# Kernel optimization log

Measured on AMD Instinct MI355X. Metric: run time of the kernel, lower is better.

## Reference

```python
import jax, jax.numpy as jnp
import numpy as np

N_HEADS = 16
D_QK = 64
D_MODEL = 1024
LN_EPS = 1e-6
B, QL, KVL = 2, 2048, 2048


def rms_norm(x, weight, eps=LN_EPS):
    var = jnp.mean(jnp.square(x.astype(jnp.float32)), axis=-1, keepdims=True)
    return (x * jax.lax.rsqrt(var + eps)).astype(x.dtype) * weight


def setup_inputs() -> dict:
    key = jax.random.key(0)
    ks = jax.random.split(key, 5)
    scale_h = 1.0 / np.sqrt(D_MODEL)
    return {
        "q_hidden_states": jax.random.normal(ks[0], (B, QL, D_MODEL), jnp.float32),
        "q_sequence_mask": jnp.ones((B, QL), dtype=bool),
        "kv_hidden_states": jax.random.normal(ks[1], (B, KVL, D_MODEL), jnp.float32),
        "kv_sequence_mask": jnp.ones((B, KVL), dtype=bool),
        "w_q": jax.random.normal(ks[2], (D_MODEL, N_HEADS * D_QK), jnp.float32) * scale_h,
        "w_kv": jax.random.normal(ks[3], (D_MODEL, 2 * N_HEADS * D_QK), jnp.float32) * scale_h,
        "w_o": jax.random.normal(ks[4], (N_HEADS * D_QK, D_MODEL), jnp.float32) * scale_h,
        "ln_weight": jnp.ones((D_MODEL,), jnp.float32),
    }


def reference(q_hidden_states, q_sequence_mask, kv_hidden_states, kv_sequence_mask,
              w_q, w_kv, w_o, ln_weight):
    b, ql, _ = q_hidden_states.shape
    kvl = kv_hidden_states.shape[1]

    normed = rms_norm(q_hidden_states, ln_weight)

    # q projection: [b, ql, H*D] -> [b, H, ql, D]
    q = (normed @ w_q).reshape(b, ql, N_HEADS, D_QK).transpose(0, 2, 1, 3)
    # kv projection: [b, kvl, 2*H*D] -> k, v each [b, H, kvl, D]
    kv = (kv_hidden_states @ w_kv).reshape(b, kvl, 2, N_HEADS, D_QK)
    k = kv[:, :, 0].transpose(0, 2, 1, 3)
    v = kv[:, :, 1].transpose(0, 2, 1, 3)

    # T5 attention: no 1/sqrt(d) scaling
    scores = jnp.einsum("bhqd,bhkd->bhqk", q, k)  # [b, H, ql, kvl]
    attn_mask = q_sequence_mask[:, None, :, None] & kv_sequence_mask[:, None, None, :]
    scores = jnp.where(attn_mask, scores, jnp.finfo(jnp.float32).min)
    attn = jax.nn.softmax(scores.astype(jnp.float32), axis=-1).astype(q.dtype)

    out = jnp.einsum("bhqk,bhkd->bhqd", attn, v)  # [b, H, ql, D]
    out = out.transpose(0, 2, 1, 3).reshape(b, ql, N_HEADS * D_QK)
    out = out @ w_o
    return q_hidden_states + out
```

## Files before the change

kernel.cpp:

```cpp
#include <hip/hip_runtime.h>
#include <stdint.h>

#define BSZ 2
#define QL 2048
#define KVL 2048
#define NH 16
#define DQK 64
#define DM 1024

typedef __bf16 bf16x8 __attribute__((ext_vector_type(8)));
typedef float f32x4 __attribute__((ext_vector_type(4)));

__device__ __forceinline__ ushort f2bf(float f) {
    union { float f; uint32_t u; } c; c.f = f;
    uint32_t u = c.u;
    return (ushort)((u + 0x7fffu + ((u >> 16) & 1u)) >> 16);
}

__device__ __forceinline__ uint32_t pack2bf(float lo, float hi) {
    union { float f; uint32_t u; } a, b;
    a.f = lo; b.f = hi;
    return __builtin_amdgcn_perm(b.u + 0x8000u, a.u + 0x8000u, 0x07060302u);
}

__device__ __forceinline__ float bflo(uint32_t w) {
    union { uint32_t u; float f; } c; c.u = w << 16; return c.f;
}
__device__ __forceinline__ float bfhi(uint32_t w) {
    union { uint32_t u; float f; } c; c.u = w & 0xffff0000u; return c.f;
}

#define GLOAD_LDS16(g, l)                                              \
    __builtin_amdgcn_global_load_lds(                                  \
        (const __attribute__((address_space(1))) uint32_t*)(g),        \
        (__attribute__((address_space(3))) uint32_t*)(l), 16, 0, 0)

__global__ __launch_bounds__(256) void prep_k(const float* __restrict__ qh_in,
                                              const float* __restrict__ lnw,
                                              ushort* __restrict__ normed,
                                              const float* __restrict__ kv_in,
                                              ushort* __restrict__ kvb,
                                              const float* __restrict__ w_q,
                                              const float* __restrict__ w_kv,
                                              const float* __restrict__ w_o,
                                              ushort* __restrict__ wqT,
                                              ushort* __restrict__ wkvT,
                                              ushort* __restrict__ woT) {
    int blk = blockIdx.x;
    int tid = threadIdx.x;
    if (blk < 4096) {
        int row = blk;
        const float4* xr = (const float4*)(qh_in + (size_t)row * DM);
        float4 v = xr[tid];
        float s = v.x * v.x + v.y * v.y + v.z * v.z + v.w * v.w;
#pragma unroll
        for (int off = 32; off > 0; off >>= 1) s += __shfl_down(s, off, 64);
        __shared__ float ws4[4];
        if ((tid & 63) == 0) ws4[tid >> 6] = s;
        __syncthreads();
        float tot = ws4[0] + ws4[1] + ws4[2] + ws4[3];
        float r = rsqrtf(tot * (1.0f / DM) + 1e-6f);
        float4 wv = ((const float4*)lnw)[tid];
        ushort4 o;
        o.x = f2bf(v.x * r * wv.x);
        o.y = f2bf(v.y * r * wv.y);
        o.z = f2bf(v.z * r * wv.z);
        o.w = f2bf(v.w * r * wv.w);
        ((ushort4*)(normed + (size_t)row * DM))[tid] = o;
        return;
    }
    if (blk < 8192) {
        int i = (blk - 4096) * 256 + tid;
        float4 v = ((const float4*)kv_in)[i];
        ushort4 r;
        r.x = f2bf(v.x); r.y = f2bf(v.y); r.z = f2bf(v.z); r.w = f2bf(v.w);
        ((ushort4*)kvb)[i] = r;
        return;
    }
    __shared__ ushort tile[64][65];
    int bi = blk - 8192;
    const float* in; ushort* out; int N, bx, by;
    const int K = 1024;
    if (bi < 256)      { in = w_q;  out = wqT;  N = 1024; bx = bi & 15; by = bi >> 4; }
    else if (bi < 768) { int j = bi - 256; in = w_kv; out = wkvT; N = 2048; bx = j & 31; by = j >> 5; }
    else               { int j = bi - 768; in = w_o;  out = woT;  N = 1024; bx = j & 15; by = j >> 4; }
    int k0 = by * 64, n0 = bx * 64;
    int colBase = tid & 63;
    int rowOff = tid >> 6;
#pragma unroll
    for (int i = 0; i < 16; ++i) {
        int row = i * 4 + rowOff;
        tile[colBase][row] = f2bf(in[(size_t)(k0 + row) * N + n0 + colBase]);
    }
    __syncthreads();
#pragma unroll
    for (int i = 0; i < 16; ++i) {
        int nrow = i * 4 + rowOff;
        out[(size_t)(n0 + nrow) * K + k0 + colBase] = tile[nrow][colBase];
    }
}

__global__ __launch_bounds__(256) void gemm_qkv_k(
    const ushort* __restrict__ normed, const ushort* __restrict__ kvb,
    const ushort* __restrict__ wqT, const ushort* __restrict__ wkvT,
    ushort* __restrict__ q_out, ushort* __restrict__ k_out, ushort* __restrict__ vt_out) {
    __shared__ __align__(16) ushort As[128 * 32];
    __shared__ __align__(16) ushort Bs[128 * 32];
    const int K = DM;
    int tid = threadIdx.x;
    int wave = tid >> 6, lane = tid & 63, quad = lane >> 4, l16 = lane & 15;
    int bx = blockIdx.x;
    int isQ = bx < 8;
    const ushort* A = isQ ? normed : kvb;
    const ushort* Bt = isQ ? wqT : wkvT;
    int n0 = (isQ ? bx : bx - 8) * 128;
    int m0 = blockIdx.y * 128;
    int wm = (wave & 1) * 64, wn = (wave >> 1) * 64;

    int r0 = tid >> 2, c0 = (tid & 3) << 3;
    const ushort* ga0 = &A[(size_t)(m0 + r0) * K + c0];
    const ushort* gb0 = &Bt[(size_t)(n0 + r0) * K + c0];

    f32x4 zero = {0.f, 0.f, 0.f, 0.f};
    f32x4 acc[4][4];
#pragma unroll
    for (int i = 0; i < 4; ++i)
#pragma unroll
        for (int j = 0; j < 4; ++j) acc[i][j] = zero;

    for (int k0 = 0; k0 < K; k0 += 32) {
        GLOAD_LDS16(ga0 + k0, &As[tid * 8]);
        GLOAD_LDS16(ga0 + (size_t)64 * K + k0, &As[(tid + 256) * 8]);
        GLOAD_LDS16(gb0 + k0, &Bs[tid * 8]);
        GLOAD_LDS16(gb0 + (size_t)64 * K + k0, &Bs[(tid + 256) * 8]);
        __syncthreads();
        bf16x8 af[4], bfr[4];
#pragma unroll
        for (int mi = 0; mi < 4; ++mi)
            af[mi] = *(const bf16x8*)(&As[(wm + mi * 16 + l16) * 32 + quad * 8]);
#pragma unroll
        for (int ni = 0; ni < 4; ++ni)
            bfr[ni] = *(const bf16x8*)(&Bs[(wn + ni * 16 + l16) * 32 + quad * 8]);
#pragma unroll
        for (int mi = 0; mi < 4; ++mi)
#pragma unroll
            for (int ni = 0; ni < 4; ++ni)
                acc[mi][ni] = __builtin_amdgcn_mfma_f32_16x16x32_bf16(
                    af[mi], bfr[ni], acc[mi][ni], 0, 0, 0);
        __syncthreads();
    }

    const float L2E = 1.44269504089f;
    if (isQ) {
        int h = (n0 + wn) >> 6;
#pragma unroll
        for (int mi = 0; mi < 4; ++mi) {
            int mm = m0 + wm + mi * 16 + quad * 4;
            int b = mm >> 11, t = mm & 2047;
            ushort* dst = &q_out[((size_t)((b << 4) | h) * QL + t) * DQK];
#pragma unroll
            for (int ni = 0; ni < 4; ++ni) {
                int d = ni * 16 + l16;
#pragma unroll
                for (int r = 0; r < 4; ++r)
                    dst[(size_t)r * DQK + d] = f2bf(acc[mi][ni][r] * L2E);
            }
        }
    } else if (((n0 + wn) >> 10) == 0) {
        int h = (n0 + wn) >> 6;
#pragma unroll
        for (int mi = 0; mi < 4; ++mi) {
            int mm = m0 + wm + mi * 16 + quad * 4;
            int b = mm >> 11, t = mm & 2047;
            ushort* dst = &k_out[((size_t)((b << 4) | h) * QL + t) * DQK];
#pragma unroll
            for (int ni = 0; ni < 4; ++ni) {
                int d = ni * 16 + l16;
#pragma unroll
                for (int r = 0; r < 4; ++r)
                    dst[(size_t)r * DQK + d] = f2bf(acc[mi][ni][r]);
            }
        }
    } else {
        int h = ((n0 + wn) >> 6) & 15;
#pragma unroll
        for (int mi = 0; mi < 4; ++mi) {
            int mm = m0 + wm + mi * 16 + quad * 4;
            int b = mm >> 11, t = mm & 2047;
#pragma unroll
            for (int ni = 0; ni < 4; ++ni) {
                int d = ni * 16 + l16;
                uint2 pk;
                pk.x = pack2bf(acc[mi][ni][0], acc[mi][ni][1]);
                pk.y = pack2bf(acc[mi][ni][2], acc[mi][ni][3]);
                *(uint2*)&vt_out[((size_t)(((b << 4) | h) * DQK + d)) * KVL + t] = pk;
            }
        }
    }
}

__global__ __launch_bounds__(256) void gemm_o_k(const ushort* __restrict__ A,
                                                const ushort* __restrict__ Bt,
                                                const float* __restrict__ resid,
                                                float* __restrict__ f_out) {
    __shared__ __align__(16) ushort As[64 * 32];
    __shared__ __align__(16) ushort Bs[128 * 32];
    const int K = DM;
    int tid = threadIdx.x;
    int wave = tid >> 6, lane = tid & 63, quad = lane >> 4, l16 = lane & 15;
    int n0 = blockIdx.x * 128, m0 = blockIdx.y * 64;
    int wm = (wave & 1) * 32, wn = (wave >> 1) * 64;

    int r0 = tid >> 2, c0 = (tid & 3) << 3;
    const ushort* ga0 = &A[(size_t)(m0 + r0) * K + c0];
    const ushort* gb0 = &Bt[(size_t)(n0 + r0) * K + c0];

    f32x4 zero = {0.f, 0.f, 0.f, 0.f};
    f32x4 acc[2][4];
#pragma unroll
    for (int i = 0; i < 2; ++i)
#pragma unroll
        for (int j = 0; j < 4; ++j) acc[i][j] = zero;

    for (int k0 = 0; k0 < K; k0 += 32) {
        GLOAD_LDS16(ga0 + k0, &As[tid * 8]);
        GLOAD_LDS16(gb0 + k0, &Bs[tid * 8]);
        GLOAD_LDS16(gb0 + (size_t)64 * K + k0, &Bs[(tid + 256) * 8]);
        __syncthreads();
        bf16x8 af[2], bfr[4];
#pragma unroll
        for (int mi = 0; mi < 2; ++mi)
            af[mi] = *(const bf16x8*)(&As[(wm + mi * 16 + l16) * 32 + quad * 8]);
#pragma unroll
        for (int ni = 0; ni < 4; ++ni)
            bfr[ni] = *(const bf16x8*)(&Bs[(wn + ni * 16 + l16) * 32 + quad * 8]);
#pragma unroll
        for (int mi = 0; mi < 2; ++mi)
#pragma unroll
            for (int ni = 0; ni < 4; ++ni)
                acc[mi][ni] = __builtin_amdgcn_mfma_f32_16x16x32_bf16(
                    af[mi], bfr[ni], acc[mi][ni], 0, 0, 0);
        __syncthreads();
    }

#pragma unroll
    for (int mi = 0; mi < 2; ++mi) {
#pragma unroll
        for (int ni = 0; ni < 4; ++ni) {
#pragma unroll
            for (int r = 0; r < 4; ++r) {
                int mm = m0 + wm + mi * 16 + quad * 4 + r;
                int nn = n0 + wn + ni * 16 + l16;
                size_t o = (size_t)mm * DM + nn;
                f_out[o] = resid[o] + acc[mi][ni][r];
            }
        }
    }
}

__global__ __launch_bounds__(256) void attn_k(const ushort* __restrict__ qh,
                                              const ushort* __restrict__ kh,
                                              const ushort* __restrict__ vt,
                                              ushort* __restrict__ o_part,
                                              float* __restrict__ l_part) {
    __shared__ __align__(16) ushort smem[2 * 64 * 72 + 8 * 16 * 72];
    ushort* Ks = smem;
    ushort* Vs = smem + 64 * 72;
    ushort* PsB = smem + 2 * 64 * 72;
    int bh = blockIdx.y;
    int q0 = blockIdx.x * 128;
    int half = blockIdx.z;
    int tbase = half * (KVL / 2);
    int tid = threadIdx.x, wave = tid >> 6, lane = tid & 63;
    int quad = lane >> 4, l16 = lane & 15;
    const ushort* Qp = qh + (size_t)bh * QL * DQK;
    const ushort* Kp = kh + (size_t)bh * KVL * DQK;
    const ushort* Vp = vt + (size_t)bh * DQK * KVL;

    bf16x8 qf[2][2];
#pragma unroll
    for (int g = 0; g < 2; ++g) {
        const ushort* qrow = Qp + (size_t)(q0 + wave * 32 + g * 16 + l16) * DQK;
        qf[g][0] = *(const bf16x8*)(qrow + quad * 8);
        qf[g][1] = *(const bf16x8*)(qrow + 32 + quad * 8);
    }

    int srow = tid >> 3;
    int scol = (tid & 7) << 3;

    f32x4 zero = {0.f, 0.f, 0.f, 0.f};
    f32x4 o[2][4];
#pragma unroll
    for (int g = 0; g < 2; ++g)
#pragma unroll
        for (int i = 0; i < 4; ++i) o[g][i] = zero;
    float lsum[2] = {0.f, 0.f};

    uint4 kr0 = *(const uint4*)&Kp[(size_t)(tbase + srow) * DQK + scol];
    uint4 kr1 = *(const uint4*)&Kp[(size_t)(tbase + srow + 32) * DQK + scol];
    uint4 vr0 = *(const uint4*)&Vp[(size_t)srow * KVL + tbase + scol];
    uint4 vr1 = *(const uint4*)&Vp[(size_t)(srow + 32) * KVL + tbase + scol];

    for (int t0 = tbase; t0 < tbase + KVL / 2; t0 += 64) {
        *(uint4*)&Ks[srow * 72 + scol] = kr0;
        *(uint4*)&Ks[(srow + 32) * 72 + scol] = kr1;
        *(uint4*)&Vs[srow * 72 + scol] = vr0;
        *(uint4*)&Vs[(srow + 32) * 72 + scol] = vr1;
        __syncthreads();
        int tn = t0 + 64;
        if (tn < tbase + KVL / 2) {
            kr0 = *(const uint4*)&Kp[(size_t)(tn + srow) * DQK + scol];
            kr1 = *(const uint4*)&Kp[(size_t)(tn + srow + 32) * DQK + scol];
            vr0 = *(const uint4*)&Vp[(size_t)srow * KVL + tn + scol];
            vr1 = *(const uint4*)&Vp[(size_t)(srow + 32) * KVL + tn + scol];
        }

        f32x4 s[2][4];
#pragma unroll
        for (int mi = 0; mi < 4; ++mi) {
            const ushort* kb = &Ks[(mi * 16 + l16) * 72 + quad * 8];
            bf16x8 kf0 = *(const bf16x8*)kb;
            bf16x8 kf1 = *(const bf16x8*)(kb + 32);
#pragma unroll
            for (int g = 0; g < 2; ++g) {
                f32x4 a = zero;
                a = __builtin_amdgcn_mfma_f32_16x16x32_bf16(kf0, qf[g][0], a, 0, 0, 0);
                a = __builtin_amdgcn_mfma_f32_16x16x32_bf16(kf1, qf[g][1], a, 0, 0, 0);
                s[g][mi] = a;
            }
        }

        bf16x8 pf[2][2];
#pragma unroll
        for (int g = 0; g < 2; ++g) {
            float rs = 0.f;
#pragma unroll
            for (int mi = 0; mi < 4; ++mi)
#pragma unroll
                for (int r = 0; r < 4; ++r) {
                    float p = __builtin_amdgcn_exp2f(s[g][mi][r]);
                    s[g][mi][r] = p;
                    rs += p;
                }
            lsum[g] += rs;
            ushort* prow = &PsB[((wave * 2 + g) * 16 + l16) * 72];
#pragma unroll
            for (int mi = 0; mi < 4; ++mi) {
                uint2 pk;
                pk.x = pack2bf(s[g][mi][0], s[g][mi][1]);
                pk.y = pack2bf(s[g][mi][2], s[g][mi][3]);
                *(uint2*)&prow[mi * 16 + quad * 4] = pk;
            }
            pf[g][0] = *(const bf16x8*)&prow[quad * 8];
            pf[g][1] = *(const bf16x8*)&prow[32 + quad * 8];
        }

#pragma unroll
        for (int mi = 0; mi < 4; ++mi) {
            const ushort* vb = &Vs[(mi * 16 + l16) * 72 + quad * 8];
            bf16x8 vf0 = *(const bf16x8*)vb;
            bf16x8 vf1 = *(const bf16x8*)(vb + 32);
#pragma unroll
            for (int g = 0; g < 2; ++g) {
                o[g][mi] = __builtin_amdgcn_mfma_f32_16x16x32_bf16(vf0, pf[g][0], o[g][mi], 0, 0, 0);
                o[g][mi] = __builtin_amdgcn_mfma_f32_16x16x32_bf16(vf1, pf[g][1], o[g][mi], 0, 0, 0);
            }
        }
        __syncthreads();
    }

#pragma unroll
    for (int g = 0; g < 2; ++g) {
        float lg = lsum[g];
        lg += __shfl_xor(lg, 16, 64);
        lg += __shfl_xor(lg, 32, 64);
        int q = q0 + wave * 32 + g * 16 + l16;
        size_t base = (size_t)(half * 32 + bh) * QL + q;
        if (quad == 0) l_part[base] = lg;
        ushort* ob = &o_part[base * DQK];
#pragma unroll
        for (int mi = 0; mi < 4; ++mi) {
            uint2 pk;
            pk.x = pack2bf(o[g][mi][0], o[g][mi][1]);
            pk.y = pack2bf(o[g][mi][2], o[g][mi][3]);
            *(uint2*)&ob[mi * 16 + quad * 4] = pk;
        }
    }
}

__global__ __launch_bounds__(256) void combine_k(const ushort* __restrict__ o_part,
                                                 const float* __restrict__ l_part,
                                                 ushort* __restrict__ attno) {
    int flat = blockIdx.x * 256 + threadIdx.x;
    int bh = flat >> 14;
    int rem = flat & 16383;
    int q = rem >> 3;
    int dc = rem & 7;
    size_t base = (size_t)bh * QL + q;
    const size_t halfStride = (size_t)32 * QL;
    float l = l_part[base] + l_part[base + halfStride];
    float rinv = __builtin_amdgcn_rcpf(l);
    const uint4 a = *(const uint4*)&o_part[base * DQK + dc * 8];
    const uint4 b = *(const uint4*)&o_part[(base + halfStride) * DQK + dc * 8];
    uint4 res;
    res.x = pack2bf((bflo(a.x) + bflo(b.x)) * rinv, (bfhi(a.x) + bfhi(b.x)) * rinv);
    res.y = pack2bf((bflo(a.y) + bflo(b.y)) * rinv, (bfhi(a.y) + bfhi(b.y)) * rinv);
    res.z = pack2bf((bflo(a.z) + bflo(b.z)) * rinv, (bfhi(a.z) + bfhi(b.z)) * rinv);
    res.w = pack2bf((bflo(a.w) + bflo(b.w)) * rinv, (bfhi(a.w) + bfhi(b.w)) * rinv);
    *(uint4*)&attno[((size_t)((bh >> 4) * QL + q)) * DM + (bh & 15) * 64 + dc * 8] = res;
}

extern "C" void kernel_launch(void* const* d_in, const int* in_sizes, int n_in,
                              void* d_out, int out_size, void* d_ws, size_t ws_size,
                              hipStream_t stream) {
    (void)in_sizes; (void)n_in; (void)out_size; (void)ws_size;
    const float* qh_in = (const float*)d_in[0];
    const float* kv_in = (const float*)d_in[2];
    const float* w_q  = (const float*)d_in[4];
    const float* w_kv = (const float*)d_in[5];
    const float* w_o  = (const float*)d_in[6];
    const float* lnw  = (const float*)d_in[7];
    float* out = (float*)d_out;

    char* ws = (char*)d_ws;
    ushort* normed = (ushort*)(ws);
    ushort* kvb    = (ushort*)(ws + ((size_t)8 << 20));
    ushort* o_part = (ushort*)(ws);
    ushort* wqT    = (ushort*)(ws + ((size_t)16 << 20));
    float*  l_part = (float*)(ws + ((size_t)16 << 20));
    ushort* wkvT   = (ushort*)(ws + ((size_t)18 << 20));
    ushort* woT    = (ushort*)(ws + ((size_t)22 << 20));
    ushort* qheads = (ushort*)(ws + ((size_t)24 << 20));
    ushort* kheads = (ushort*)(ws + ((size_t)32 << 20));
    ushort* vT     = (ushort*)(ws + ((size_t)40 << 20));
    ushort* attno  = (ushort*)(ws + ((size_t)48 << 20));

    prep_k<<<9216, 256, 0, stream>>>(qh_in, lnw, normed, kv_in, kvb,
                                     w_q, w_kv, w_o, wqT, wkvT, woT);
    gemm_qkv_k<<<dim3(24, 32), 256, 0, stream>>>(normed, kvb, wqT, wkvT,
                                                 qheads, kheads, vT);
    attn_k<<<dim3(QL / 128, BSZ * NH, 2), 256, 0, stream>>>(qheads, kheads, vT,
                                                            o_part, l_part);
    combine_k<<<2048, 256, 0, stream>>>(o_part, l_part, attno);
    gemm_o_k<<<dim3(8, 64), 256, 0, stream>>>(attno, woT, qh_in, out);
}
```

Measured before the change: 226.5 us.

## Load K/V fragments directly from global in attention and coalesce V-transpose stores

The attention kernel drops the shared-memory K/V staging and both block barriers. Each wave now owns 64 query rows and reads its K and V MFMA fragments straight from global memory (through L1/L2), keeping only a per-wave P buffer in LDS. The grid is flattened to 512 blocks with launch bounds requesting two blocks per CU. Separately, the QKV GEMM epilogue stages the V tile through LDS so the transposed V writes become 16-byte coalesced stores instead of scattered 8-byte writes. The trade-off is more global and cache traffic, since each wave fetches K/V on its own, and higher register pressure from the larger per-wave accumulators.

```diff
diff --git a/kernel.cpp b/kernel.cpp
--- a/kernel.cpp
+++ b/kernel.cpp
@@ -104,8 +104,9 @@
     const ushort* __restrict__ normed, const ushort* __restrict__ kvb,
     const ushort* __restrict__ wqT, const ushort* __restrict__ wkvT,
     ushort* __restrict__ q_out, ushort* __restrict__ k_out, ushort* __restrict__ vt_out) {
-    __shared__ __align__(16) ushort As[128 * 32];
-    __shared__ __align__(16) ushort Bs[128 * 32];
+    __shared__ __align__(16) ushort smem[16896];
+    ushort* As = smem;
+    ushort* Bs = smem + 4096;
     const int K = DM;
     int tid = threadIdx.x;
     int wave = tid >> 6, lane = tid & 63, quad = lane >> 4, l16 = lane & 15;
@@ -166,7 +167,7 @@
                     dst[(size_t)r * DQK + d] = f2bf(acc[mi][ni][r] * L2E);
             }
         }
-    } else if (((n0 + wn) >> 10) == 0) {
+    } else if ((n0 >> 10) == 0) {
         int h = (n0 + wn) >> 6;
 #pragma unroll
         for (int mi = 0; mi < 4; ++mi) {
@@ -182,19 +183,29 @@
             }
         }
     } else {
-        int h = ((n0 + wn) >> 6) & 15;
+        int b = m0 >> 11;
+        int m0t = m0 & 2047;
+        int hbase = (n0 >> 6) & 15;
+        int rbase = ((b << 4) | hbase) * 64;
 #pragma unroll
         for (int mi = 0; mi < 4; ++mi) {
-            int mm = m0 + wm + mi * 16 + quad * 4;
-            int b = mm >> 11, t = mm & 2047;
+            int t_loc = wm + mi * 16 + quad * 4;
 #pragma unroll
             for (int ni = 0; ni < 4; ++ni) {
-                int d = ni * 16 + l16;
+                int n_loc = wn + ni * 16 + l16;
                 uint2 pk;
                 pk.x = pack2bf(acc[mi][ni][0], acc[mi][ni][1]);
                 pk.y = pack2bf(acc[mi][ni][2], acc[mi][ni][3]);
-                *(uint2*)&vt_out[((size_t)(((b << 4) | h) * DQK + d)) * KVL + t] = pk;
-            }
+                *(uint2*)&smem[n_loc * 132 + t_loc] = pk;
+            }
+        }
+        __syncthreads();
+#pragma unroll
+        for (int it = 0; it < 8; ++it) {
+            int idx = it * 256 + tid;
+            int n = idx >> 4, ch = (idx & 15) << 3;
+            uint4 vv = *(const uint4*)&smem[n * 132 + ch];
+            *(uint4*)&vt_out[((size_t)(rbase + n)) * KVL + m0t + ch] = vv;
         }
     }
 }
@@ -258,123 +269,97 @@
     }
 }
 
-__global__ __launch_bounds__(256) void attn_k(const ushort* __restrict__ qh,
-                                              const ushort* __restrict__ kh,
-                                              const ushort* __restrict__ vt,
-                                              ushort* __restrict__ o_part,
-                                              float* __restrict__ l_part) {
-    __shared__ __align__(16) ushort smem[2 * 64 * 72 + 8 * 16 * 72];
-    ushort* Ks = smem;
-    ushort* Vs = smem + 64 * 72;
-    ushort* PsB = smem + 2 * 64 * 72;
-    int bh = blockIdx.y;
-    int q0 = blockIdx.x * 128;
-    int half = blockIdx.z;
-    int tbase = half * (KVL / 2);
+__global__ __launch_bounds__(256, 2) void attn_k(const ushort* __restrict__ qh,
+                                                 const ushort* __restrict__ kh,
+                                                 const ushort* __restrict__ vt,
+                                                 ushort* __restrict__ o_part,
+                                                 float* __restrict__ l_part) {
+    __shared__ __align__(16) ushort Ps[4][16 * 72];
     int tid = threadIdx.x, wave = tid >> 6, lane = tid & 63;
     int quad = lane >> 4, l16 = lane & 15;
+    int bx = blockIdx.x;
+    int bh = bx >> 4;
+    int half = (bx >> 3) & 1;
+    int q0 = ((bx & 7) * 4 + wave) * 64;
+    int tbase = half * (KVL / 2);
     const ushort* Qp = qh + (size_t)bh * QL * DQK;
     const ushort* Kp = kh + (size_t)bh * KVL * DQK;
     const ushort* Vp = vt + (size_t)bh * DQK * KVL;
 
-    bf16x8 qf[2][2];
-#pragma unroll
-    for (int g = 0; g < 2; ++g) {
-        const ushort* qrow = Qp + (size_t)(q0 + wave * 32 + g * 16 + l16) * DQK;
+    bf16x8 qf[4][2];
+#pragma unroll
+    for (int g = 0; g < 4; ++g) {
+        const ushort* qrow = Qp + (size_t)(q0 + g * 16 + l16) * DQK;
         qf[g][0] = *(const bf16x8*)(qrow + quad * 8);
         qf[g][1] = *(const bf16x8*)(qrow + 32 + quad * 8);
     }
 
-    int srow = tid >> 3;
-    int scol = (tid & 7) << 3;
-
     f32x4 zero = {0.f, 0.f, 0.f, 0.f};
-    f32x4 o[2][4];
-#pragma unroll
-    for (int g = 0; g < 2; ++g)
+    f32x4 o[4][4];
+#pragma unroll
+    for (int g = 0; g < 4; ++g)
 #pragma unroll
         for (int i = 0; i < 4; ++i) o[g][i] = zero;
-    float lsum[2] = {0.f, 0.f};
-
-    uint4 kr0 = *(const uint4*)&Kp[(size_t)(tbase + srow) * DQK + scol];
-    uint4 kr1 = *(const uint4*)&Kp[(size_t)(tbase + srow + 32) * DQK + scol];
-    uint4 vr0 = *(const uint4*)&Vp[(size_t)srow * KVL + tbase + scol];
-    uint4 vr1 = *(const uint4*)&Vp[(size_t)(srow + 32) * KVL + tbase + scol];
-
-    for (int t0 = tbase; t0 < tbase + KVL / 2; t0 += 64) {
-        *(uint4*)&Ks[srow * 72 + scol] = kr0;
-        *(uint4*)&Ks[(srow + 32) * 72 + scol] = kr1;
-        *(uint4*)&Vs[srow * 72 + scol] = vr0;
-        *(uint4*)&Vs[(srow + 32) * 72 + scol] = vr1;
-        __syncthreads();
-        int tn = t0 + 64;
-        if (tn < tbase + KVL / 2) {
-            kr0 = *(const uint4*)&Kp[(size_t)(tn + srow) * DQK + scol];
-            kr1 = *(const uint4*)&Kp[(size_t)(tn + srow + 32) * DQK + scol];
-            vr0 = *(const uint4*)&Vp[(size_t)srow * KVL + tn + scol];
-            vr1 = *(const uint4*)&Vp[(size_t)(srow + 32) * KVL + tn + scol];
-        }
-
-        f32x4 s[2][4];
+    float lsum[4] = {0.f, 0.f, 0.f, 0.f};
+
+    ushort* prow = &Ps[wave][l16 * 72];
+    const ushort* kbase = Kp + (size_t)(tbase + l16) * DQK + quad * 8;
+    const ushort* vbase = Vp + (size_t)l16 * KVL + tbase + quad * 8;
+
+    for (int ti = 0; ti < (KVL / 2) / 64; ++ti) {
+        bf16x8 kf[4][2], vf[4][2];
 #pragma unroll
         for (int mi = 0; mi < 4; ++mi) {
-            const ushort* kb = &Ks[(mi * 16 + l16) * 72 + quad * 8];
-            bf16x8 kf0 = *(const bf16x8*)kb;
-            bf16x8 kf1 = *(const bf16x8*)(kb + 32);
-#pragma unroll
-            for (int g = 0; g < 2; ++g) {
+            const ushort* kb = kbase + ((size_t)ti * 64 + mi * 16) * DQK;
+            kf[mi][0] = *(const bf16x8*)kb;
+            kf[mi][1] = *(const bf16x8*)(kb + 32);
+            const ushort* vb = vbase + (size_t)(mi * 16) * KVL + ti * 64;
+            vf[mi][0] = *(const bf16x8*)vb;
+            vf[mi][1] = *(const bf16x8*)(vb + 32);
+        }
+#pragma unroll
+        for (int g = 0; g < 4; ++g) {
+            f32x4 s[4];
+#pragma unroll
+            for (int mi = 0; mi < 4; ++mi) {
                 f32x4 a = zero;
-                a = __builtin_amdgcn_mfma_f32_16x16x32_bf16(kf0, qf[g][0], a, 0, 0, 0);
-                a = __builtin_amdgcn_mfma_f32_16x16x32_bf16(kf1, qf[g][1], a, 0, 0, 0);
-                s[g][mi] = a;
-            }
-        }
-
-        bf16x8 pf[2][2];
-#pragma unroll
-        for (int g = 0; g < 2; ++g) {
+                a = __builtin_amdgcn_mfma_f32_16x16x32_bf16(kf[mi][0], qf[g][0], a, 0, 0, 0);
+                a = __builtin_amdgcn_mfma_f32_16x16x32_bf16(kf[mi][1], qf[g][1], a, 0, 0, 0);
+                s[mi] = a;
+            }
             float rs = 0.f;
 #pragma unroll
             for (int mi = 0; mi < 4; ++mi)
 #pragma unroll
                 for (int r = 0; r < 4; ++r) {
-                    float p = __builtin_amdgcn_exp2f(s[g][mi][r]);
-                    s[g][mi][r] = p;
+                    float p = __builtin_amdgcn_exp2f(s[mi][r]);
+                    s[mi][r] = p;
                     rs += p;
                 }
             lsum[g] += rs;
-            ushort* prow = &PsB[((wave * 2 + g) * 16 + l16) * 72];
 #pragma unroll
             for (int mi = 0; mi < 4; ++mi) {
                 uint2 pk;
-                pk.x = pack2bf(s[g][mi][0], s[g][mi][1]);
-                pk.y = pack2bf(s[g][mi][2], s[g][mi][3]);
+                pk.x = pack2bf(s[mi][0], s[mi][1]);
+                pk.y = pack2bf(s[mi][2], s[mi][3]);
                 *(uint2*)&prow[mi * 16 + quad * 4] = pk;
             }
-            pf[g][0] = *(const bf16x8*)&prow[quad * 8];
-            pf[g][1] = *(const bf16x8*)&prow[32 + quad * 8];
-        }
-
-#pragma unroll
-        for (int mi = 0; mi < 4; ++mi) {
-            const ushort* vb = &Vs[(mi * 16 + l16) * 72 + quad * 8];
-            bf16x8 vf0 = *(const bf16x8*)vb;
-            bf16x8 vf1 = *(const bf16x8*)(vb + 32);
-#pragma unroll
-            for (int g = 0; g < 2; ++g) {
-                o[g][mi] = __builtin_amdgcn_mfma_f32_16x16x32_bf16(vf0, pf[g][0], o[g][mi], 0, 0, 0);
-                o[g][mi] = __builtin_amdgcn_mfma_f32_16x16x32_bf16(vf1, pf[g][1], o[g][mi], 0, 0, 0);
-            }
-        }
-        __syncthreads();
-    }
-
-#pragma unroll
-    for (int g = 0; g < 2; ++g) {
+            bf16x8 pf0 = *(const bf16x8*)&prow[quad * 8];
+            bf16x8 pf1 = *(const bf16x8*)&prow[32 + quad * 8];
+#pragma unroll
+            for (int mi = 0; mi < 4; ++mi) {
+                o[g][mi] = __builtin_amdgcn_mfma_f32_16x16x32_bf16(vf[mi][0], pf0, o[g][mi], 0, 0, 0);
+                o[g][mi] = __builtin_amdgcn_mfma_f32_16x16x32_bf16(vf[mi][1], pf1, o[g][mi], 0, 0, 0);
+            }
+        }
+    }
+
+#pragma unroll
+    for (int g = 0; g < 4; ++g) {
         float lg = lsum[g];
         lg += __shfl_xor(lg, 16, 64);
         lg += __shfl_xor(lg, 32, 64);
-        int q = q0 + wave * 32 + g * 16 + l16;
+        int q = q0 + g * 16 + l16;
         size_t base = (size_t)(half * 32 + bh) * QL + q;
         if (quad == 0) l_part[base] = lg;
         ushort* ob = &o_part[base * DQK];
@@ -439,8 +424,7 @@
                                      w_q, w_kv, w_o, wqT, wkvT, woT);
     gemm_qkv_k<<<dim3(24, 32), 256, 0, stream>>>(normed, kvb, wqT, wkvT,
                                                  qheads, kheads, vT);
-    attn_k<<<dim3(QL / 128, BSZ * NH, 2), 256, 0, stream>>>(qheads, kheads, vT,
-                                                            o_part, l_part);
+    attn_k<<<512, 256, 0, stream>>>(qheads, kheads, vT, o_part, l_part);
     combine_k<<<2048, 256, 0, stream>>>(o_part, l_part, attno);
     gemm_o_k<<<dim3(8, 64), 256, 0, stream>>>(attno, woT, qh_in, out);
 }
```

New measurement: 244.9 us. +8.1%, slower.
